# Performance work log

Measured on AMD Instinct MI355X. Metric: run time of the kernel, lower is better.

Reference implementation:

```python
import jax, jax.numpy as jnp
import numpy as np

M, N, D = 2048, 131072, 256

def setup_inputs() -> dict:
    key = jax.random.key(0)
    kq, kv = jax.random.split(key)
    query = jax.random.normal(kq, (M, D), dtype=jnp.float32)
    vectors = jax.random.normal(kv, (N, D), dtype=jnp.float32)
    return {"query": query, "vectors": vectors}

def reference(query, vectors):
    # torch.cdist(query, vectors, p=2).argmin(dim=1)
    # Euclidean distance via ||q||^2 + ||v||^2 - 2 q.v (GEMM-based, same math)
    q_sq = jnp.sum(query * query, axis=-1, keepdims=True)        # [M,1]
    v_sq = jnp.sum(vectors * vectors, axis=-1)                    # [N]
    cross = jnp.einsum('md,nd->mn', query, vectors)               # [M,N]
    dist_sq = jnp.maximum(q_sq + v_sq[None, :] - 2.0 * cross, 0.0)
    # sqrt is monotonic so argmin(dist) == argmin(dist_sq); take sqrt for faithfulness
    dist = jnp.sqrt(dist_sq)
    return jnp.argmin(dist, axis=1)                               # [M] int
```

## Files before the change

### kernel.cpp

```cpp
#include <hip/hip_runtime.h>

#define M 2048
#define N 131072
#define D 256

#define SLICE_G 64
#define NSLICE  (N / (SLICE_G * 16))
#define GEN     8
#define NGEN    (SLICE_G / GEN)
#define NQBLK   4
#define BIAS    1024.0f

typedef __attribute__((ext_vector_type(8))) _Float16 half8;
typedef __attribute__((ext_vector_type(8))) short short8;
typedef __attribute__((ext_vector_type(4))) float f32x4;
typedef unsigned long long ull;

__device__ __forceinline__ ull pack_key(float score, unsigned idx) {
    unsigned u = __float_as_uint(score);
    u = (u & 0x80000000u) ? ~u : (u | 0x80000000u);
    return ((ull)u << 32) | idx;
}

__global__ __launch_bounds__(512, 2) void dist_argmin_fused(const float* __restrict__ q,
                                                            const float* __restrict__ v,
                                                            ull* __restrict__ keys1,
                                                            ull* __restrict__ keys2) {
    __shared__ short bt[2][GEN][8 * 512];
    __shared__ float vsq_s[2][GEN][16][8];

    const int tid  = threadIdx.x;
    const int lane = tid & 63;
    const int w    = tid >> 6;
    const int tx   = lane & 15;
    const int quad = (lane >> 4) & 3;

    const int lb    = blockIdx.x;
    const int xcd   = lb & 7;
    const int s_    = lb >> 3;
    const int slice = xcd * 16 + (s_ >> 2);
    const int qblk  = s_ & 3;

    const int qb0 = qblk * 512 + w * 64;
    const int sg0 = slice * SLICE_G;

    half8 aq[4][8];
#pragma unroll
    for (int mt = 0; mt < 4; ++mt) {
        const float* qrow = q + (size_t)(qb0 + mt * 16 + tx) * 256 + quad * 8;
#pragma unroll
        for (int c = 0; c < 8; ++c) {
            const float4 f0 = *(const float4*)(qrow + c * 32);
            const float4 f1 = *(const float4*)(qrow + c * 32 + 4);
            half8 hh;
            hh[0] = (_Float16)f0.x; hh[1] = (_Float16)f0.y;
            hh[2] = (_Float16)f0.z; hh[3] = (_Float16)f0.w;
            hh[4] = (_Float16)f1.x; hh[5] = (_Float16)f1.y;
            hh[6] = (_Float16)f1.z; hh[7] = (_Float16)f1.w;
            aq[mt][c] = hh;
        }
    }

    unsigned best[16];
#pragma unroll
    for (int i = 0; i < 16; ++i) best[i] = 0xFFFFFFFFu;

    const float* vp = v + ((size_t)sg0 * 16 + tx) * 256 + w * 32 + quad * 8;

    auto cvtwrite = [&](int buf, int t, const float4& f0, const float4& f1) {
        float s = f0.x * f0.x + f0.y * f0.y + f0.z * f0.z + f0.w * f0.w;
        s = fmaf(f1.x, f1.x, s); s = fmaf(f1.y, f1.y, s);
        s = fmaf(f1.z, f1.z, s); s = fmaf(f1.w, f1.w, s);
        half8 h;
        h[0] = (_Float16)f0.x; h[1] = (_Float16)f0.y;
        h[2] = (_Float16)f0.z; h[3] = (_Float16)f0.w;
        h[4] = (_Float16)f1.x; h[5] = (_Float16)f1.y;
        h[6] = (_Float16)f1.z; h[7] = (_Float16)f1.w;
        *(short8*)&bt[buf][t][w * 512 + lane * 8] = *(short8*)&h;
        s += __shfl_xor(s, 16, 64);
        s += __shfl_xor(s, 32, 64);
        if (lane < 16) vsq_s[buf][t][lane][w] = s;
    };

    auto compute = [&](int buf, int t, int g) {
        const float4 p0 = *(const float4*)&vsq_s[buf][t][tx][0];
        const float4 p1 = *(const float4*)&vsq_s[buf][t][tx][4];
        const float vsqr = ((p0.x + p0.y) + (p0.z + p0.w))
                         + ((p1.x + p1.y) + (p1.z + p1.w)) + BIAS;
        f32x4 acc[4];
#pragma unroll
        for (int i = 0; i < 4; ++i) acc[i] = (f32x4){0.f, 0.f, 0.f, 0.f};
        __builtin_amdgcn_s_setprio(1);
#pragma unroll
        for (int c = 0; c < 8; ++c) {
            const half8 b = *(const half8*)&bt[buf][t][c * 512 + lane * 8];
#pragma unroll
            for (int mt = 0; mt < 4; ++mt)
                acc[mt] = __builtin_amdgcn_mfma_f32_16x16x32_f16(aq[mt][c], b, acc[mt], 0, 0, 0);
        }
        __builtin_amdgcn_s_setprio(0);
#pragma unroll
        for (int mt = 0; mt < 4; ++mt)
#pragma unroll
            for (int r = 0; r < 4; ++r) {
                const float sc = fmaf(-2.f, acc[mt][r], vsqr);
                const unsigned key = (__float_as_uint(sc) & 0xFFFFFFC0u) | (unsigned)g;
                const int sl = mt * 4 + r;
                best[sl] = key < best[sl] ? key : best[sl];
            }
    };

    for (int t = 0; t < GEN; t += 2) {
        const float* p0 = vp + (size_t)t * 4096;
        const float* p1 = vp + (size_t)(t + 1) * 4096;
        const float4 a0 = *(const float4*)p0;
        const float4 a1 = *(const float4*)(p0 + 4);
        const float4 b0 = *(const float4*)p1;
        const float4 b1 = *(const float4*)(p1 + 4);
        cvtwrite(0, t, a0, a1);
        cvtwrite(0, t + 1, b0, b1);
    }
    __syncthreads();

    int buf = 0;
    for (int gen = 0; gen < NGEN; ++gen) {
        const int gbase = gen * GEN;
        if (gen + 1 < NGEN) {
            for (int t = 0; t < GEN; ++t) {
                const float* p = vp + (size_t)(gbase + GEN + t) * 4096;
                const float4 f0 = *(const float4*)p;
                const float4 f1 = *(const float4*)(p + 4);
                compute(buf, t, gbase + t);
                cvtwrite(buf ^ 1, t, f0, f1);
            }
        } else {
            for (int t = 0; t < GEN; ++t) compute(buf, t, gbase + t);
        }
        __syncthreads();
        buf ^= 1;
    }

#pragma unroll
    for (int mt = 0; mt < 4; ++mt)
#pragma unroll
        for (int r = 0; r < 4; ++r) {
            const int sl = mt * 4 + r;
            unsigned k = best[sl];
#pragma unroll
            for (int off = 8; off; off >>= 1) {
                const unsigned o = (unsigned)__shfl_xor((int)k, off, 16);
                k = o < k ? o : k;
            }
            const ull bal = __ballot(best[sl] == k);
            const unsigned grp = (unsigned)((bal >> (quad * 16)) & 0xFFFFull);
            const int wtx = __ffs((int)grp) - 1;
            const unsigned n = (unsigned)((sg0 + (int)(k & 63u)) * 16 + wtx);
            if (tx == 0) {
                const int row = qb0 + mt * 16 + quad * 4 + r;
                const ull key64 = ((ull)k << 32) | n;
                const ull old = atomicMin(&keys1[row], key64);
                const ull loser = (key64 < old) ? old : key64;
                if (loser != ~0ull) atomicMin(&keys2[row], loser);
            }
        }
}

__global__ __launch_bounds__(256) void rescore_kernel(const float* __restrict__ q,
                                                      const float* __restrict__ v,
                                                      const ull* __restrict__ keys1,
                                                      const ull* __restrict__ keys2,
                                                      int* __restrict__ out) {
    const int qi   = blockIdx.x * 4 + (threadIdx.x >> 6);
    const int lane = threadIdx.x & 63;
    const float4 qv = *(const float4*)(q + (size_t)qi * D + lane * 4);
    ull best = ~0ull;
    ull cand[2];
    cand[0] = keys1[qi];
    cand[1] = keys2[qi];
#pragma unroll
    for (int c = 0; c < 2; ++c) {
        if (cand[c] == ~0ull) continue;
        const unsigned idx = (unsigned)cand[c];
        const float4 vv = *(const float4*)(v + (size_t)idx * D + lane * 4);
        float s1 = vv.x * vv.x + vv.y * vv.y + vv.z * vv.z + vv.w * vv.w;
        float s2 = qv.x * vv.x + qv.y * vv.y + qv.z * vv.z + qv.w * vv.w;
#pragma unroll
        for (int off = 32; off; off >>= 1) {
            s1 += __shfl_xor(s1, off, 64);
            s2 += __shfl_xor(s2, off, 64);
        }
        const float dist = fmaf(-2.0f, s2, s1);
        const ull key = pack_key(dist, idx);
        best = best < key ? best : key;
    }
    if (lane == 0) out[qi] = (int)(unsigned)(best & 0xFFFFFFFFull);
}

extern "C" void kernel_launch(void* const* d_in, const int* in_sizes, int n_in,
                              void* d_out, int out_size, void* d_ws, size_t ws_size,
                              hipStream_t stream) {
    const float* q = (const float*)d_in[0];
    const float* v = (const float*)d_in[1];
    int* out = (int*)d_out;

    ull* keys1 = (ull*)d_ws;
    ull* keys2 = keys1 + M;

    hipMemsetAsync(d_ws, 0xFF, (size_t)2 * M * sizeof(ull), stream);

    dist_argmin_fused<<<NQBLK * NSLICE, 512, 0, stream>>>(q, v, keys1, keys2);

    rescore_kernel<<<M / 4, 256, 0, stream>>>(q, v, keys1, keys2, out);
}
```

Measured before the change: 386.7 us.

## Halve waves per block, double query rows per wave, pre-convert queries to fp16

Each block now runs 4 waves of 256 threads instead of 8, and each wave handles 128 query rows (8 MFMA row tiles) instead of 64. Every staged vector fragment read from LDS therefore feeds twice as many MFMAs, and each wave loads and converts two 32-element chunks of the vector tile. A separate q_convert kernel writes the queries as fp16 in MFMA fragment order to the workspace, so the main kernel loads them directly. In exchange, register use rises sharply (64 half8 query fragments, 32 running minima, 8 accumulators), occupancy drops to one block per CU, and there is an extra kernel launch.

```diff
diff --git a/kernel.cpp b/kernel.cpp
--- a/kernel.cpp
+++ b/kernel.cpp
@@ -22,12 +22,37 @@
     return ((ull)u << 32) | idx;
 }
 
-__global__ __launch_bounds__(512, 2) void dist_argmin_fused(const float* __restrict__ q,
+__global__ __launch_bounds__(256) void q_convert(const float* __restrict__ q,
+                                                 short* __restrict__ qf) {
+    const int g    = blockIdx.x;
+    const int t    = threadIdx.x;
+    const int w    = t >> 6;
+    const int l    = t & 63;
+    const int quad = (l >> 4) & 3;
+    const int tx   = l & 15;
+
+    const float* src = q + (size_t)g * 4096;
+#pragma unroll
+    for (int h = 0; h < 2; ++h) {
+        const int c = w + h * 4;
+        const float* p = src + tx * 256 + c * 32 + quad * 8;
+        const float4 f0 = *(const float4*)p;
+        const float4 f1 = *(const float4*)(p + 4);
+        half8 hh;
+        hh[0] = (_Float16)f0.x; hh[1] = (_Float16)f0.y;
+        hh[2] = (_Float16)f0.z; hh[3] = (_Float16)f0.w;
+        hh[4] = (_Float16)f1.x; hh[5] = (_Float16)f1.y;
+        hh[6] = (_Float16)f1.z; hh[7] = (_Float16)f1.w;
+        *(short8*)(qf + ((size_t)g * 8 + c) * 512 + l * 8) = *(short8*)&hh;
+    }
+}
+
+__global__ __launch_bounds__(256, 1) void dist_argmin_fused(const short* __restrict__ qf,
                                                             const float* __restrict__ v,
                                                             ull* __restrict__ keys1,
                                                             ull* __restrict__ keys2) {
     __shared__ short bt[2][GEN][8 * 512];
-    __shared__ float vsq_s[2][GEN][16][8];
+    __shared__ float vsq_s[2][GEN][16][4];
 
     const int tid  = threadIdx.x;
     const int lane = tid & 63;
@@ -41,42 +66,42 @@
     const int slice = xcd * 16 + (s_ >> 2);
     const int qblk  = s_ & 3;
 
-    const int qb0 = qblk * 512 + w * 64;
+    const int qb0 = qblk * 512 + w * 128;
     const int sg0 = slice * SLICE_G;
 
-    half8 aq[4][8];
-#pragma unroll
-    for (int mt = 0; mt < 4; ++mt) {
-        const float* qrow = q + (size_t)(qb0 + mt * 16 + tx) * 256 + quad * 8;
-#pragma unroll
-        for (int c = 0; c < 8; ++c) {
-            const float4 f0 = *(const float4*)(qrow + c * 32);
-            const float4 f1 = *(const float4*)(qrow + c * 32 + 4);
-            half8 hh;
-            hh[0] = (_Float16)f0.x; hh[1] = (_Float16)f0.y;
-            hh[2] = (_Float16)f0.z; hh[3] = (_Float16)f0.w;
-            hh[4] = (_Float16)f1.x; hh[5] = (_Float16)f1.y;
-            hh[6] = (_Float16)f1.z; hh[7] = (_Float16)f1.w;
-            aq[mt][c] = hh;
-        }
-    }
-
-    unsigned best[16];
-#pragma unroll
-    for (int i = 0; i < 16; ++i) best[i] = 0xFFFFFFFFu;
-
-    const float* vp = v + ((size_t)sg0 * 16 + tx) * 256 + w * 32 + quad * 8;
-
-    auto cvtwrite = [&](int buf, int t, const float4& f0, const float4& f1) {
-        float s = f0.x * f0.x + f0.y * f0.y + f0.z * f0.z + f0.w * f0.w;
-        s = fmaf(f1.x, f1.x, s); s = fmaf(f1.y, f1.y, s);
-        s = fmaf(f1.z, f1.z, s); s = fmaf(f1.w, f1.w, s);
-        half8 h;
-        h[0] = (_Float16)f0.x; h[1] = (_Float16)f0.y;
-        h[2] = (_Float16)f0.z; h[3] = (_Float16)f0.w;
-        h[4] = (_Float16)f1.x; h[5] = (_Float16)f1.y;
-        h[6] = (_Float16)f1.z; h[7] = (_Float16)f1.w;
-        *(short8*)&bt[buf][t][w * 512 + lane * 8] = *(short8*)&h;
+    half8 aq[8][8];
+#pragma unroll
+    for (int mt = 0; mt < 8; ++mt)
+#pragma unroll
+        for (int c = 0; c < 8; ++c)
+            aq[mt][c] = *(const half8*)(qf + ((size_t)((qb0 >> 4) + mt) * 8 + c) * 512 + lane * 8);
+
+    unsigned best[32];
+#pragma unroll
+    for (int i = 0; i < 32; ++i) best[i] = 0xFFFFFFFFu;
+
+    const float* vp = v + ((size_t)sg0 * 16 + tx) * 256 + w * 64 + quad * 8;
+
+    auto cvtwrite = [&](int buf, int t, const float4& f00, const float4& f01,
+                        const float4& f10, const float4& f11) {
+        float s = f00.x * f00.x + f00.y * f00.y + f00.z * f00.z + f00.w * f00.w;
+        s = fmaf(f01.x, f01.x, s); s = fmaf(f01.y, f01.y, s);
+        s = fmaf(f01.z, f01.z, s); s = fmaf(f01.w, f01.w, s);
+        s = fmaf(f10.x, f10.x, s); s = fmaf(f10.y, f10.y, s);
+        s = fmaf(f10.z, f10.z, s); s = fmaf(f10.w, f10.w, s);
+        s = fmaf(f11.x, f11.x, s); s = fmaf(f11.y, f11.y, s);
+        s = fmaf(f11.z, f11.z, s); s = fmaf(f11.w, f11.w, s);
+        half8 h0, h1;
+        h0[0] = (_Float16)f00.x; h0[1] = (_Float16)f00.y;
+        h0[2] = (_Float16)f00.z; h0[3] = (_Float16)f00.w;
+        h0[4] = (_Float16)f01.x; h0[5] = (_Float16)f01.y;
+        h0[6] = (_Float16)f01.z; h0[7] = (_Float16)f01.w;
+        h1[0] = (_Float16)f10.x; h1[1] = (_Float16)f10.y;
+        h1[2] = (_Float16)f10.z; h1[3] = (_Float16)f10.w;
+        h1[4] = (_Float16)f11.x; h1[5] = (_Float16)f11.y;
+        h1[6] = (_Float16)f11.z; h1[7] = (_Float16)f11.w;
+        *(short8*)&bt[buf][t][(2 * w) * 512 + lane * 8]     = *(short8*)&h0;
+        *(short8*)&bt[buf][t][(2 * w + 1) * 512 + lane * 8] = *(short8*)&h1;
         s += __shfl_xor(s, 16, 64);
         s += __shfl_xor(s, 32, 64);
         if (lane < 16) vsq_s[buf][t][lane][w] = s;
@@ -84,23 +109,21 @@
 
     auto compute = [&](int buf, int t, int g) {
         const float4 p0 = *(const float4*)&vsq_s[buf][t][tx][0];
-        const float4 p1 = *(const float4*)&vsq_s[buf][t][tx][4];
-        const float vsqr = ((p0.x + p0.y) + (p0.z + p0.w))
-                         + ((p1.x + p1.y) + (p1.z + p1.w)) + BIAS;
-        f32x4 acc[4];
-#pragma unroll
-        for (int i = 0; i < 4; ++i) acc[i] = (f32x4){0.f, 0.f, 0.f, 0.f};
+        const float vsqr = ((p0.x + p0.y) + (p0.z + p0.w)) + BIAS;
+        f32x4 acc[8];
+#pragma unroll
+        for (int i = 0; i < 8; ++i) acc[i] = (f32x4){0.f, 0.f, 0.f, 0.f};
         __builtin_amdgcn_s_setprio(1);
 #pragma unroll
         for (int c = 0; c < 8; ++c) {
             const half8 b = *(const half8*)&bt[buf][t][c * 512 + lane * 8];
 #pragma unroll
-            for (int mt = 0; mt < 4; ++mt)
+            for (int mt = 0; mt < 8; ++mt)
                 acc[mt] = __builtin_amdgcn_mfma_f32_16x16x32_f16(aq[mt][c], b, acc[mt], 0, 0, 0);
         }
         __builtin_amdgcn_s_setprio(0);
 #pragma unroll
-        for (int mt = 0; mt < 4; ++mt)
+        for (int mt = 0; mt < 8; ++mt)
 #pragma unroll
             for (int r = 0; r < 4; ++r) {
                 const float sc = fmaf(-2.f, acc[mt][r], vsqr);
@@ -110,15 +133,14 @@
             }
     };
 
-    for (int t = 0; t < GEN; t += 2) {
-        const float* p0 = vp + (size_t)t * 4096;
-        const float* p1 = vp + (size_t)(t + 1) * 4096;
-        const float4 a0 = *(const float4*)p0;
-        const float4 a1 = *(const float4*)(p0 + 4);
-        const float4 b0 = *(const float4*)p1;
-        const float4 b1 = *(const float4*)(p1 + 4);
-        cvtwrite(0, t, a0, a1);
-        cvtwrite(0, t + 1, b0, b1);
+#pragma unroll 1
+    for (int t = 0; t < GEN; ++t) {
+        const float* p = vp + (size_t)t * 4096;
+        const float4 f00 = *(const float4*)p;
+        const float4 f01 = *(const float4*)(p + 4);
+        const float4 f10 = *(const float4*)(p + 32);
+        const float4 f11 = *(const float4*)(p + 36);
+        cvtwrite(0, t, f00, f01, f10, f11);
     }
     __syncthreads();
 
@@ -126,14 +148,18 @@
     for (int gen = 0; gen < NGEN; ++gen) {
         const int gbase = gen * GEN;
         if (gen + 1 < NGEN) {
+#pragma unroll 1
             for (int t = 0; t < GEN; ++t) {
                 const float* p = vp + (size_t)(gbase + GEN + t) * 4096;
-                const float4 f0 = *(const float4*)p;
-                const float4 f1 = *(const float4*)(p + 4);
+                const float4 f00 = *(const float4*)p;
+                const float4 f01 = *(const float4*)(p + 4);
+                const float4 f10 = *(const float4*)(p + 32);
+                const float4 f11 = *(const float4*)(p + 36);
                 compute(buf, t, gbase + t);
-                cvtwrite(buf ^ 1, t, f0, f1);
+                cvtwrite(buf ^ 1, t, f00, f01, f10, f11);
             }
         } else {
+#pragma unroll 1
             for (int t = 0; t < GEN; ++t) compute(buf, t, gbase + t);
         }
         __syncthreads();
@@ -141,7 +167,7 @@
     }
 
 #pragma unroll
-    for (int mt = 0; mt < 4; ++mt)
+    for (int mt = 0; mt < 8; ++mt)
 #pragma unroll
         for (int r = 0; r < 4; ++r) {
             const int sl = mt * 4 + r;
@@ -205,10 +231,13 @@
 
     ull* keys1 = (ull*)d_ws;
     ull* keys2 = keys1 + M;
+    short* qf = (short*)(keys2 + M);
 
     hipMemsetAsync(d_ws, 0xFF, (size_t)2 * M * sizeof(ull), stream);
 
-    dist_argmin_fused<<<NQBLK * NSLICE, 512, 0, stream>>>(q, v, keys1, keys2);
+    q_convert<<<M / 16, 256, 0, stream>>>(q, qf);
+
+    dist_argmin_fused<<<NQBLK * NSLICE, 256, 0, stream>>>(qf, v, keys1, keys2);
 
     rescore_kernel<<<M / 4, 256, 0, stream>>>(q, v, keys1, keys2, out);
 }
```

Result: slower. 418.7 us (+8.3%).
